# Kernel optimization log

Measured on AMD Instinct MI355X. Metric: run time of the kernel, lower is better.

Reference implementation:

```python
import jax, jax.numpy as jnp
import numpy as np

N, F, D = 4096, 32, 16      # nodes, channels, irrep dim for L<=3 (1+3+5+7)
E = 65536                    # edges (avg degree 16)
S = 64                       # species
R = 8                        # radial basis size
AVG = 16.0                   # avg_num_neighbors
L_SLICES = ((0, 1), (1, 4), (4, 9), (9, 16))   # per-l blocks of the 16-dim irrep axis
IR_OUT_REPS = np.array([1, 3])                 # output irreps 0e (dim 1) + 1o (dim 3)
MIX_REPS = np.array([1, 3, 5, 7])              # per-l scalar mix broadcast over m


def _sph(v):
    # real spherical harmonics l=1..3 of normalized vectors (4pi-normalized), [E,15]
    r2 = jnp.sum(v * v, axis=-1, keepdims=True)
    u = v / jnp.sqrt(jnp.where(r2 == 0.0, 1.0, r2))
    x, y, z = u[:, 0], u[:, 1], u[:, 2]
    s3, s5, s7 = 3.0 ** 0.5, 5.0 ** 0.5, 7.0 ** 0.5
    s15, s42, s70, s105 = 15.0 ** 0.5, 42.0 ** 0.5, 70.0 ** 0.5, 105.0 ** 0.5
    Y1 = [s3 * x, s3 * y, s3 * z]
    Y2 = [s15 * x * y, s15 * y * z, 0.5 * s5 * (3 * z * z - 1), s15 * x * z, 0.5 * s15 * (x * x - y * y)]
    Y3 = [0.25 * s70 * y * (3 * x * x - y * y), s105 * x * y * z, 0.25 * s42 * y * (5 * z * z - 1),
          0.5 * s7 * z * (5 * z * z - 3), 0.25 * s42 * x * (5 * z * z - 1),
          0.5 * s105 * z * (x * x - y * y), 0.25 * s70 * x * (x * x - 3 * y * y)]
    return jnp.stack(Y1 + Y2 + Y3, axis=-1)


def _per_l_linear(xs, W):
    # channel mixing within each l block: xs [N,C,16], W [4,C,Fout] -> [N,Fout,16]
    return jnp.concatenate([jnp.einsum('nci,cf->nfi', xs[:, :, a:b], W[l])
                            for l, (a, b) in enumerate(L_SLICES)], axis=-1)


def setup_inputs() -> dict:
    key = jax.random.key(0)
    ks = jax.random.split(key, 17)
    rs = np.random.RandomState(0)
    # sparse CG-like tensor-product / symmetric-contraction basis tensors (fixed constants)
    cg = (rs.randn(D, 15, D) * (rs.rand(D, 15, D) < 0.08)).astype(np.float32)
    u3 = (rs.randn(D, D, D, 4) * (rs.rand(D, D, D, 4) < 0.05)).astype(np.float32)
    u2 = (rs.randn(D, D, 4) * (rs.rand(D, D, 4) < 0.15)).astype(np.float32)
    u1 = (rs.randn(D, 4) * (rs.rand(D, 4) < 0.4)).astype(np.float32)

    def g(k, shape, s):
        return jax.random.normal(k, shape, dtype=jnp.float32) * s

    return {
        'node_feats': g(ks[0], (N, F, D), 1.0),
        'vectors': g(ks[1], (E, 3), 1.0),
        'radial_embedding': jax.random.uniform(ks[2], (E, R), dtype=jnp.float32),
        'W_up': g(ks[3], (4, F, F), F ** -0.5),
        'CG': jnp.asarray(cg),
        'W_r1': g(ks[4], (R, 64), R ** -0.5),
        'W_r2': g(ks[5], (64, 64), 64 ** -0.5),
        'W_r3': g(ks[6], (64, 64), 64 ** -0.5),
        'W_r4': g(ks[7], (64, 2 * F * 4), 64 ** -0.5),
        'W_down': g(ks[8], (4, 2 * F, F), (2 * F) ** -0.5),
        'U3': jnp.asarray(u3),
        'U2': jnp.asarray(u2),
        'U1': jnp.asarray(u1),
        'w3': g(ks[9], (S, 2, F), 1.0),
        'w2': g(ks[10], (S, 2, F), 1.0),
        'w1': g(ks[11], (S, 2, F), 1.0),
        'W_sc': g(ks[12], (2, S, F, F), F ** -0.5),
        'W_out': g(ks[13], (2, F, F), F ** -0.5),
        'node_species': jax.random.randint(ks[14], (N,), 0, S, dtype=jnp.int32),
        'senders': jax.random.randint(ks[15], (E,), 0, N, dtype=jnp.int32),
        'receivers': jax.random.randint(ks[16], (E,), 0, N, dtype=jnp.int32),
    }


def _forward(node_feats, vectors, radial_embedding, W_up, CG, W_r1, W_r2, W_r3, W_r4,
             W_down, U3, U2, U1, w3, w2, w1, W_sc, W_out,
             node_species, senders, receivers):
    # linear_up
    x = _per_l_linear(node_feats, W_up)                              # [N,F,16]
    # message passing convolution
    fs = x[senders]                                                  # gather [E,F,16]
    Y = _sph(vectors)                                                # [E,15]
    M = jnp.einsum('ej,ijk->eik', Y, CG)                             # per-edge TP operator [E,16,16]
    tp = jnp.einsum('efi,eik->efk', fs, M)                           # [E,F,16]
    msg = jnp.concatenate([fs, tp], axis=1)                          # [E,2F,16]
    h = jax.nn.silu(radial_embedding @ W_r1)
    h = jax.nn.silu(h @ W_r2)
    h = jax.nn.silu(h @ W_r3)
    mix = (h @ W_r4).reshape(E, 2 * F, 4)                            # per-(channel,l) scalar
    mix = jnp.repeat(mix, MIX_REPS, axis=-1, total_repeat_length=D)  # [E,2F,16]
    msg = msg * mix
    agg = jax.ops.segment_sum(msg, receivers, num_segments=N) / jnp.sqrt(AVG)
    y = _per_l_linear(agg, W_down) / jnp.sqrt(AVG)                   # linear_down [N,F,16]
    # symmetric contraction (correlation 3) with species-indexed weights
    def expand(w):  # [S,2,F] -> per-node per-output-irrep-dim scalar [N,F,4]
        return jnp.repeat(jnp.transpose(w[node_species], (0, 2, 1)), IR_OUT_REPS,
                          axis=-1, total_repeat_length=4)
    w3e, w2e, w1e = expand(w3), expand(w2), expand(w1)
    T = jnp.einsum('abji,ncj->ncabi', U3, y) * w3e[:, :, None, None, :]  # [N,F,16,16,4]
    T = T + U2[None, None] * w2e[:, :, None, None, :]
    T = jnp.einsum('ncaji,ncj->ncai', T, y)                              # [N,F,16,4]
    T = T + U1[None, None] * w1e[:, :, None, :]
    B = jnp.einsum('ncji,ncj->nci', T, y)                                # [N,F,4]
    # output linear (per output irrep) + species-indexed skip connection
    o = jnp.concatenate([jnp.einsum('nci,cf->nfi', B[:, :, :1], W_out[0]),
                         jnp.einsum('nci,cf->nfi', B[:, :, 1:4], W_out[1])], axis=-1)
    sc = jnp.concatenate([jnp.einsum('nci,ncf->nfi', x[:, :, :1], W_sc[0][node_species]),
                          jnp.einsum('nci,ncf->nfi', x[:, :, 1:4], W_sc[1][node_species])], axis=-1)
    return (o + sc).reshape(N, F * 4)


def reference(node_feats, vectors, radial_embedding, W_up, CG, W_r1, W_r2, W_r3, W_r4,
              W_down, U3, U2, U1, w3, w2, w1, W_sc, W_out,
              node_species, senders, receivers):
    return _forward(node_feats, vectors, radial_embedding, W_up, CG, W_r1, W_r2, W_r3, W_r4,
                    W_down, U3, U2, U1, w3, w2, w1, W_sc, W_out,
                    node_species, senders, receivers)
```

## Files before the change

kernel.cpp:

```cpp
#include <hip/hip_runtime.h>
#include <math.h>

#define NN 4096
#define FF 32
#define DD 16
#define EE 65536

__device__ __forceinline__ int l_of(int i){ return (i==0)?0:(i<4)?1:(i<9)?2:3; }
__device__ __forceinline__ float silu(float v){ return v/(1.f+expf(-v)); }

__global__ __launch_bounds__(512) void k_x(const float* __restrict__ feats,
        const float* __restrict__ Wup, float* __restrict__ x){
  __shared__ float sF[FF*DD];
  __shared__ float sW[4*FF*FF];
  int n = blockIdx.x, t = threadIdx.x;
  sF[t] = feats[(size_t)n*FF*DD + t];
  for (int k=t;k<4*FF*FF;k+=512) sW[k]=Wup[k];
  __syncthreads();
  int f = t>>4, i = t&15;
  const float* W = &sW[l_of(i)*FF*FF];
  float a=0.f;
  #pragma unroll
  for (int c=0;c<FF;c++) a += sF[c*DD+i]*W[c*FF+f];
  x[(size_t)n*FF*DD + t] = a;
}

__global__ __launch_bounds__(256) void k_Y(const float* __restrict__ vec, float* __restrict__ Yp){
  int e = blockIdx.x*256+threadIdx.x;
  if (e>=EE) return;
  float vx=vec[(size_t)e*3+0], vy=vec[(size_t)e*3+1], vz=vec[(size_t)e*3+2];
  float r2=vx*vx+vy*vy+vz*vz;
  float inv = (r2==0.f)?1.f:rsqrtf(r2);
  float X=vx*inv, Y=vy*inv, Z=vz*inv;
  const float s3=1.7320508075688772f, s5=2.23606797749979f, s7=2.6457513110645907f;
  const float s15=3.872983346207417f, s42=6.48074069840786f, s70=8.366600265340756f, s105=10.246950765959598f;
  float y[16];
  y[0]=s3*X; y[1]=s3*Y; y[2]=s3*Z;
  y[3]=s15*X*Y; y[4]=s15*Y*Z; y[5]=0.5f*s5*(3.f*Z*Z-1.f); y[6]=s15*X*Z; y[7]=0.5f*s15*(X*X-Y*Y);
  y[8]=0.25f*s70*Y*(3.f*X*X-Y*Y); y[9]=s105*X*Y*Z; y[10]=0.25f*s42*Y*(5.f*Z*Z-1.f);
  y[11]=0.5f*s7*Z*(5.f*Z*Z-3.f); y[12]=0.25f*s42*X*(5.f*Z*Z-1.f);
  y[13]=0.5f*s105*Z*(X*X-Y*Y); y[14]=0.25f*s70*X*(X*X-3.f*Y*Y);
  y[15]=0.f;
  #pragma unroll
  for(int q=0;q<4;q++) *(float4*)&Yp[(size_t)e*16+q*4] = *(float4*)&y[q*4];
}

__global__ __launch_bounds__(256) void k_mix(const float* __restrict__ rad,
    const float* __restrict__ W1, const float* __restrict__ W2,
    const float* __restrict__ W3, const float* __restrict__ W4,
    float* __restrict__ mix){
  __shared__ float sRadT[8*68];
  __shared__ float sW1[8*64];
  __shared__ float sHA[64*68];
  __shared__ float sHB[64*68];
  int t = threadIdx.x;
  int be = blockIdx.x*64;
  for (int k=t;k<8*64;k+=256) sW1[k]=W1[k];
  for (int idx=t; idx<64*8; idx+=256){ int e=idx>>3, k=idx&7; sRadT[k*68+e]=rad[(size_t)(be+e)*8+k]; }
  __syncthreads();
  int e0 = (t>>4)*4, j0 = (t&15)*4;
  {
    float acc[4][4];
    #pragma unroll
    for(int a=0;a<4;a++){ acc[a][0]=0;acc[a][1]=0;acc[a][2]=0;acc[a][3]=0; }
    #pragma unroll
    for(int k=0;k<8;k++){
      float4 h = *(const float4*)&sRadT[k*68+e0];
      float4 w = *(const float4*)&sW1[k*64+j0];
      acc[0][0]+=h.x*w.x; acc[0][1]+=h.x*w.y; acc[0][2]+=h.x*w.z; acc[0][3]+=h.x*w.w;
      acc[1][0]+=h.y*w.x; acc[1][1]+=h.y*w.y; acc[1][2]+=h.y*w.z; acc[1][3]+=h.y*w.w;
      acc[2][0]+=h.z*w.x; acc[2][1]+=h.z*w.y; acc[2][2]+=h.z*w.z; acc[2][3]+=h.z*w.w;
      acc[3][0]+=h.w*w.x; acc[3][1]+=h.w*w.y; acc[3][2]+=h.w*w.z; acc[3][3]+=h.w*w.w;
    }
    #pragma unroll
    for(int b=0;b<4;b++){
      float4 v; v.x=silu(acc[0][b]); v.y=silu(acc[1][b]); v.z=silu(acc[2][b]); v.w=silu(acc[3][b]);
      *(float4*)&sHA[(j0+b)*68+e0] = v;
    }
  }
  __syncthreads();
  {
    float acc[4][4];
    #pragma unroll
    for(int a=0;a<4;a++){ acc[a][0]=0;acc[a][1]=0;acc[a][2]=0;acc[a][3]=0; }
    for(int k=0;k<64;k++){
      float4 h = *(const float4*)&sHA[k*68+e0];
      float4 w = *(const float4*)&W2[k*64+j0];
      acc[0][0]+=h.x*w.x; acc[0][1]+=h.x*w.y; acc[0][2]+=h.x*w.z; acc[0][3]+=h.x*w.w;
      acc[1][0]+=h.y*w.x; acc[1][1]+=h.y*w.y; acc[1][2]+=h.y*w.z; acc[1][3]+=h.y*w.w;
      acc[2][0]+=h.z*w.x; acc[2][1]+=h.z*w.y; acc[2][2]+=h.z*w.z; acc[2][3]+=h.z*w.w;
      acc[3][0]+=h.w*w.x; acc[3][1]+=h.w*w.y; acc[3][2]+=h.w*w.z; acc[3][3]+=h.w*w.w;
    }
    #pragma unroll
    for(int b=0;b<4;b++){
      float4 v; v.x=silu(acc[0][b]); v.y=silu(acc[1][b]); v.z=silu(acc[2][b]); v.w=silu(acc[3][b]);
      *(float4*)&sHB[(j0+b)*68+e0] = v;
    }
  }
  __syncthreads();
  {
    float acc[4][4];
    #pragma unroll
    for(int a=0;a<4;a++){ acc[a][0]=0;acc[a][1]=0;acc[a][2]=0;acc[a][3]=0; }
    for(int k=0;k<64;k++){
      float4 h = *(const float4*)&sHB[k*68+e0];
      float4 w = *(const float4*)&W3[k*64+j0];
      acc[0][0]+=h.x*w.x; acc[0][1]+=h.x*w.y; acc[0][2]+=h.x*w.z; acc[0][3]+=h.x*w.w;
      acc[1][0]+=h.y*w.x; acc[1][1]+=h.y*w.y; acc[1][2]+=h.y*w.z; acc[1][3]+=h.y*w.w;
      acc[2][0]+=h.z*w.x; acc[2][1]+=h.z*w.y; acc[2][2]+=h.z*w.z; acc[2][3]+=h.z*w.w;
      acc[3][0]+=h.w*w.x; acc[3][1]+=h.w*w.y; acc[3][2]+=h.w*w.z; acc[3][3]+=h.w*w.w;
    }
    #pragma unroll
    for(int b=0;b<4;b++){
      float4 v; v.x=silu(acc[0][b]); v.y=silu(acc[1][b]); v.z=silu(acc[2][b]); v.w=silu(acc[3][b]);
      *(float4*)&sHA[(j0+b)*68+e0] = v;
    }
  }
  __syncthreads();
  {
    int cc0 = (t&63)*4, g = t>>6;
    float acc[4][4][4];
    #pragma unroll
    for(int r=0;r<4;r++)
      #pragma unroll
      for(int a=0;a<4;a++){ acc[r][a][0]=0;acc[r][a][1]=0;acc[r][a][2]=0;acc[r][a][3]=0; }
    for(int k=0;k<64;k++){
      float4 w = *(const float4*)&W4[k*256+cc0];
      #pragma unroll
      for(int r=0;r<4;r++){
        float4 h = *(const float4*)&sHA[k*68 + (g+4*r)*4];
        acc[r][0][0]+=h.x*w.x; acc[r][0][1]+=h.x*w.y; acc[r][0][2]+=h.x*w.z; acc[r][0][3]+=h.x*w.w;
        acc[r][1][0]+=h.y*w.x; acc[r][1][1]+=h.y*w.y; acc[r][1][2]+=h.y*w.z; acc[r][1][3]+=h.y*w.w;
        acc[r][2][0]+=h.z*w.x; acc[r][2][1]+=h.z*w.y; acc[r][2][2]+=h.z*w.z; acc[r][2][3]+=h.z*w.w;
        acc[r][3][0]+=h.w*w.x; acc[r][3][1]+=h.w*w.y; acc[r][3][2]+=h.w*w.z; acc[r][3][3]+=h.w*w.w;
      }
    }
    #pragma unroll
    for(int r=0;r<4;r++)
      #pragma unroll
      for(int a=0;a<4;a++){
        int e = (g+4*r)*4 + a;
        float4 v; v.x=acc[r][a][0]; v.y=acc[r][a][1]; v.z=acc[r][a][2]; v.w=acc[r][a][3];
        *(float4*)&mix[(size_t)(be+e)*256 + cc0] = v;
      }
  }
}

__global__ void k_zero(int* cnt){ int t=blockIdx.x*256+threadIdx.x; if(t<NN) cnt[t]=0; }
__global__ void k_count(const int* __restrict__ recv, int* cnt, int* pos){
  int e=blockIdx.x*256+threadIdx.x; pos[e]=atomicAdd(&cnt[recv[e]],1); }
__global__ __launch_bounds__(256) void k_scan(const int* __restrict__ cnt, int* __restrict__ off){
  __shared__ int sums[256]; __shared__ int bases[256];
  int t=threadIdx.x;
  int local[16]; int s=0;
  #pragma unroll
  for(int k=0;k<16;k++){ local[k]=cnt[t*16+k]; s+=local[k]; }
  sums[t]=s; __syncthreads();
  if(t==0){ int a=0; for(int q=0;q<256;q++){ bases[q]=a; a+=sums[q]; } }
  __syncthreads();
  int acc=bases[t];
  #pragma unroll
  for(int k=0;k<16;k++){ off[t*16+k]=acc; acc+=local[k]; }
  if(t==255) off[NN]=acc;
}
__global__ void k_fill(const int* __restrict__ recv, const int* __restrict__ off,
                       const int* __restrict__ pos, int* __restrict__ elist){
  int e=blockIdx.x*256+threadIdx.x; elist[off[recv[e]]+pos[e]]=e; }

__global__ __launch_bounds__(256) void k_compact(const float* __restrict__ U3,
    const float* __restrict__ U2, const float* __restrict__ U1,
    int* u3i, float* u3v, int* u2i, float* u2v, int* u1i, float* u1v, int* uoff){
  const float* src; int n; int* oi; float* ov; int slot=blockIdx.x;
  if(slot==0){src=U3;n=16384;oi=u3i;ov=u3v;}
  else if(slot==1){src=U2;n=1024;oi=u2i;ov=u2v;}
  else {src=U1;n=64;oi=u1i;ov=u1v;}
  __shared__ int cnts[256][4]; __shared__ int bases[256][4];
  int t=threadIdx.x;
  int chunk=(n+255)/256;
  int lo=t*chunk, hi=min(n,lo+chunk); if(lo>n) lo=n;
  int c0=0,c1=0,c2=0,c3=0;
  for(int q=lo;q<hi;q++) if(src[q]!=0.f){
    int i=q&3;
    if(i==0)c0++; else if(i==1)c1++; else if(i==2)c2++; else c3++;
  }
  cnts[t][0]=c0; cnts[t][1]=c1; cnts[t][2]=c2; cnts[t][3]=c3;
  __syncthreads();
  if(t==0){
    int a=0;
    for(int i=0;i<4;i++){ uoff[slot*5+i]=a;
      for(int q=0;q<256;q++){ bases[q][i]=a; a+=cnts[q][i]; } }
    uoff[slot*5+4]=a;
  }
  __syncthreads();
  int w0=bases[t][0], w1_=bases[t][1], w2_=bases[t][2], w3_=bases[t][3];
  for(int q=lo;q<hi;q++){ float v=src[q]; if(v!=0.f){
    int i=q&3;
    if(i==0){ oi[w0]=q; ov[w0]=v; w0++; }
    else if(i==1){ oi[w1_]=q; ov[w1_]=v; w1_++; }
    else if(i==2){ oi[w2_]=q; ov[w2_]=v; w2_++; }
    else { oi[w3_]=q; ov[w3_]=v; w3_++; }
  } }
}

__global__ __launch_bounds__(256) void k_gather(
    const float* __restrict__ x, const float* __restrict__ mix,
    const float* __restrict__ Yp, const float* __restrict__ CG,
    const int* __restrict__ senders,
    const int* __restrict__ off, const int* __restrict__ elist,
    float* __restrict__ agg)
{
  __shared__ __align__(16) char smem[22528];
  float* sCG  = (float*)smem;
  float* sMW  = (float*)(smem+15360);
  float* sP   = (float*)smem;
  int*   sEl  = (int*)(smem+19456);
  int*   sEl2 = (int*)(smem+20480);
  int*   sSnd = (int*)(smem+21504);

  int n = blockIdx.x, t = threadIdx.x;
  int w = t>>6, l = t&63, lc = l&31, kh = (l>>5)*8;

  for (int k=t;k<3840;k+=256) sCG[k]=CG[k];
  int base = off[n];
  int deg = off[n+1]-base; if (deg>256) deg=256;
  for (int d=t; d<deg; d+=256) sEl[d]=elist[base+d];
  __syncthreads();
  for (int d=t; d<deg; d+=256){
    int v=sEl[d]; int r=0;
    for(int q=0;q<deg;q++) r += (sEl[q]<v);
    sEl2[r]=v;
  }
  __syncthreads();
  for (int d=t; d<deg; d+=256) sSnd[d]=senders[sEl2[d]];
  __syncthreads();

  float aggF[8], aggT[8];
  #pragma unroll
  for(int j=0;j<8;j++){ aggF[j]=0.f; aggT[j]=0.f; }

  for (int g0=0; g0<deg; g0+=4){
    int d = g0+w;
    if (d<deg){
      int myE = __builtin_amdgcn_readfirstlane(sEl2[d]);
      int snd = __builtin_amdgcn_readfirstlane(sSnd[d]);
      const float* yrow = Yp + (size_t)myE*16;
      const float* mrow = mix + (size_t)myE*256;
      const float* xrow = x + (size_t)snd*512;
      float yv[16];
      #pragma unroll
      for(int q=0;q<4;q++) *(float4*)&yv[q*4] = *(const float4*)&yrow[q*4];
      float4 mixF = *(const float4*)&mrow[lc*4];
      float4 mixT = *(const float4*)&mrow[128 + lc*4];
      float fsv[16];
      #pragma unroll
      for(int q=0;q<4;q++) *(float4*)&fsv[q*4] = *(const float4*)&xrow[lc*16 + q*4];
      int li = l>>4, lk = l&15;
      #pragma unroll
      for(int r=0;r<4;r++){
        int i = r*4+li;
        float m=0.f;
        #pragma unroll
        for(int j=0;j<15;j++) m += yv[j]*sCG[i*240 + j*16 + lk];
        sMW[w*256 + r*64 + l] = m;
      }
      float tp[8];
      #pragma unroll
      for(int j=0;j<8;j++) tp[j]=0.f;
      #pragma unroll
      for(int i=0;i<16;i++){
        float4 ma = *(const float4*)&sMW[w*256 + i*16 + kh];
        float4 mb = *(const float4*)&sMW[w*256 + i*16 + kh + 4];
        float f = fsv[i];
        tp[0]+=f*ma.x; tp[1]+=f*ma.y; tp[2]+=f*ma.z; tp[3]+=f*ma.w;
        tp[4]+=f*mb.x; tp[5]+=f*mb.y; tp[6]+=f*mb.z; tp[7]+=f*mb.w;
      }
      #pragma unroll
      for(int j=0;j<8;j++){
        int k = kh+j;
        int g = l_of(k);
        float mF = (g==0)?mixF.x:(g==1)?mixF.y:(g==2)?mixF.z:mixF.w;
        float mT = (g==0)?mixT.x:(g==1)?mixT.y:(g==2)?mixT.z:mixT.w;
        aggF[j] += fsv[k]*mF;
        aggT[j] += tp[j]*mT;
      }
    }
  }
  __syncthreads();

  #pragma unroll
  for(int j=0;j<8;j++){
    sP[w*1024 + lc*16 + kh + j]       = aggF[j];
    sP[w*1024 + (32+lc)*16 + kh + j]  = aggT[j];
  }
  __syncthreads();
  for (int idx=t; idx<1024; idx+=256)
    agg[(size_t)n*1024 + idx] = sP[idx]+sP[1024+idx]+sP[2048+idx]+sP[3072+idx];
}

__global__ __launch_bounds__(256) void k_tail(
    const float* __restrict__ agg, const float* __restrict__ x,
    const float* __restrict__ Wdown,
    const int* __restrict__ u3i, const float* __restrict__ u3v,
    const int* __restrict__ u2i, const float* __restrict__ u2v,
    const int* __restrict__ u1i, const float* __restrict__ u1v,
    const int* __restrict__ uoff,
    const float* __restrict__ w3, const float* __restrict__ w2,
    const float* __restrict__ w1,
    const float* __restrict__ Wsc, const float* __restrict__ Wout,
    const int* __restrict__ species,
    float* __restrict__ out)
{
  __shared__ float sAgg[2048];
  __shared__ float sy[1024];
  __shared__ float sPart[1024];

  int n0 = blockIdx.x*2, t = threadIdx.x;
  #pragma unroll
  for(int q=0;q<8;q++) sAgg[q*256+t] = agg[(size_t)n0*1024 + q*256 + t];
  __syncthreads();

  {
    int h=t>>7, ii=(t>>3)&15, f0=(t&7)*4;
    const float* W = Wdown + l_of(ii)*2048;
    float ax=0.f, ay=0.f, az=0.f, aw=0.f;
    for(int c=0;c<64;c++){
      float a = sAgg[h*1024 + c*16 + ii];
      float4 wv = *(const float4*)&W[c*32+f0];
      ax+=a*wv.x; ay+=a*wv.y; az+=a*wv.z; aw+=a*wv.w;
    }
    sy[h*512 + ii*32 + f0+0]=ax*0.0625f;
    sy[h*512 + ii*32 + f0+1]=ay*0.0625f;
    sy[h*512 + ii*32 + f0+2]=az*0.0625f;
    sy[h*512 + ii*32 + f0+3]=aw*0.0625f;
  }
  __syncthreads();

  float* sXn = sAgg;
  float* sB  = sAgg + 1024;
  #pragma unroll
  for(int q=0;q<4;q++){ int idx=q*256+t;
    sXn[idx] = x[(size_t)(n0+(idx>>9))*512 + (idx&511)]; }

  {
    int p  = __builtin_amdgcn_readfirstlane(t>>6);
    int c  = t&31, hf=(t>>5)&1;
    int spec = species[n0+hf];
    const float* syc = &sy[hf*512 + c];
    #pragma unroll
    for(int i=0;i<4;i++){
      float r3=0.f;
      for(int q=uoff[i]+p; q<uoff[i+1]; q+=4){
        int id=u3i[q]; float v=u3v[q];
        int a=(id>>10)&15, b=(id>>6)&15, j=(id>>2)&15;
        r3 += v*syc[a*32]*syc[b*32]*syc[j*32];
      }
      float r2=0.f;
      for(int q=uoff[5+i]+p; q<uoff[5+i+1]; q+=4){
        int id=u2i[q]; float v=u2v[q];
        int a=(id>>6)&15, b=(id>>2)&15;
        r2 += v*syc[a*32]*syc[b*32];
      }
      float r1=0.f;
      for(int q=uoff[10+i]+p; q<uoff[10+i+1]; q+=4){
        int id=u1i[q]; float v=u1v[q];
        int a=(id>>2)&15;
        r1 += v*syc[a*32];
      }
      float wa = (i==0)? w3[spec*64+c] : w3[spec*64+32+c];
      float wb = (i==0)? w2[spec*64+c] : w2[spec*64+32+c];
      float wc = (i==0)? w1[spec*64+c] : w1[spec*64+32+c];
      sPart[p*256 + i*64 + hf*32 + c] = r3*wa + r2*wb + r1*wc;
    }
  }
  __syncthreads();

  {
    int hf2=t>>7, c2=(t>>2)&31, i2=t&3;
    int o = i2*64 + hf2*32 + c2;
    sB[hf2*128 + c2*4 + i2] = sPart[o] + sPart[256+o] + sPart[512+o] + sPart[768+o];
  }
  __syncthreads();

  {
    int hf3=t>>7, f=(t>>2)&31, i3=t&3;
    int sp2 = species[n0+hf3];
    int sel = (i3==0)?0:1;
    const float* Wo = Wout + sel*1024;
    const float* Ws = Wsc + (size_t)(sel*64+sp2)*1024;
    float o=0.f, sc=0.f;
    for(int c2=0;c2<32;c2++){
      o  += sB[hf3*128 + c2*4 + i3]*Wo[c2*32+f];
      sc += sXn[hf3*512 + c2*16 + i3]*Ws[c2*32+f];
    }
    out[(size_t)(n0+hf3)*128 + f*4 + i3] = o + sc;
  }
}

extern "C" void kernel_launch(void* const* d_in, const int* in_sizes, int n_in,
                              void* d_out, int out_size, void* d_ws, size_t ws_size,
                              hipStream_t stream){
  (void)in_sizes; (void)n_in; (void)out_size; (void)ws_size;
  const float* feats = (const float*)d_in[0];
  const float* vec   = (const float*)d_in[1];
  const float* rad   = (const float*)d_in[2];
  const float* Wup   = (const float*)d_in[3];
  const float* CG    = (const float*)d_in[4];
  const float* Wr1   = (const float*)d_in[5];
  const float* Wr2   = (const float*)d_in[6];
  const float* Wr3   = (const float*)d_in[7];
  const float* Wr4   = (const float*)d_in[8];
  const float* Wdown = (const float*)d_in[9];
  const float* U3    = (const float*)d_in[10];
  const float* U2    = (const float*)d_in[11];
  const float* U1    = (const float*)d_in[12];
  const float* w3    = (const float*)d_in[13];
  const float* w2    = (const float*)d_in[14];
  const float* w1    = (const float*)d_in[15];
  const float* Wsc   = (const float*)d_in[16];
  const float* Wout  = (const float*)d_in[17];
  const int* species = (const int*)d_in[18];
  const int* senders = (const int*)d_in[19];
  const int* recv    = (const int*)d_in[20];
  float* out = (float*)d_out;

  char* w = (char*)d_ws;
  float* x    = (float*)w;  w += (size_t)NN*512*4;
  float* mix  = (float*)w;  w += (size_t)EE*256*4;
  float* Yp   = (float*)w;  w += (size_t)EE*16*4;
  float* agg  = (float*)w;  w += (size_t)NN*1024*4;
  int* cnt    = (int*)w;    w += (size_t)NN*4;
  int* off    = (int*)w;    w += (size_t)(NN+1)*4;
  int* pos    = (int*)w;    w += (size_t)EE*4;
  int* elist  = (int*)w;    w += (size_t)EE*4;
  int* u3i    = (int*)w;    w += 16384*4;
  float* u3v  = (float*)w;  w += 16384*4;
  int* u2i    = (int*)w;    w += 1024*4;
  float* u2v  = (float*)w;  w += 1024*4;
  int* u1i    = (int*)w;    w += 64*4;
  float* u1v  = (float*)w;  w += 64*4;
  int* uoff   = (int*)w;    w += 16*4;

  k_compact<<<3,256,0,stream>>>(U3,U2,U1,u3i,u3v,u2i,u2v,u1i,u1v,uoff);
  k_x<<<NN,512,0,stream>>>(feats,Wup,x);
  k_Y<<<EE/256,256,0,stream>>>(vec,Yp);
  k_mix<<<EE/64,256,0,stream>>>(rad,Wr1,Wr2,Wr3,Wr4,mix);
  k_zero<<<NN/256,256,0,stream>>>(cnt);
  k_count<<<EE/256,256,0,stream>>>(recv,cnt,pos);
  k_scan<<<1,256,0,stream>>>(cnt,off);
  k_fill<<<EE/256,256,0,stream>>>(recv,off,pos,elist);
  k_gather<<<NN,256,0,stream>>>(x,mix,Yp,CG,senders,off,elist,agg);
  k_tail<<<NN/2,256,0,stream>>>(agg,x,Wdown,u3i,u3v,u2i,u2v,u1i,u1v,uoff,
                                w3,w2,w1,Wsc,Wout,species,out);
}
```

Measured before the change: 315.4 us.

## Write edge data in receiver-sorted order and give each wave its own node in gather

A new sort kernel computes each edge's position in the receiver-sorted, edge-id-ordered list and the sender for that slot. The Y and mix kernels then scatter their outputs into that order, so the gather reads mix and Y rows contiguously. The gather kernel now assigns one node per wavefront (four nodes per block) instead of splitting one node's edges across four waves. This removes the in-block rank sort, the shared-memory reduction and the per-block syncs. The costs are an extra kernel and scattered writes in k_Y and k_mix, and low-degree nodes may leave waves less evenly loaded.

```diff
diff --git a/kernel.cpp b/kernel.cpp
--- a/kernel.cpp
+++ b/kernel.cpp
@@ -25,7 +25,8 @@
   x[(size_t)n*FF*DD + t] = a;
 }
 
-__global__ __launch_bounds__(256) void k_Y(const float* __restrict__ vec, float* __restrict__ Yp){
+__global__ __launch_bounds__(256) void k_Y(const float* __restrict__ vec,
+        const int* __restrict__ epos, float* __restrict__ Yp){
   int e = blockIdx.x*256+threadIdx.x;
   if (e>=EE) return;
   float vx=vec[(size_t)e*3+0], vy=vec[(size_t)e*3+1], vz=vec[(size_t)e*3+2];
@@ -41,14 +42,15 @@
   y[11]=0.5f*s7*Z*(5.f*Z*Z-3.f); y[12]=0.25f*s42*X*(5.f*Z*Z-1.f);
   y[13]=0.5f*s105*Z*(X*X-Y*Y); y[14]=0.25f*s70*X*(X*X-3.f*Y*Y);
   y[15]=0.f;
-  #pragma unroll
-  for(int q=0;q<4;q++) *(float4*)&Yp[(size_t)e*16+q*4] = *(float4*)&y[q*4];
+  size_t ep = (size_t)epos[e];
+  #pragma unroll
+  for(int q=0;q<4;q++) *(float4*)&Yp[ep*16+q*4] = *(float4*)&y[q*4];
 }
 
 __global__ __launch_bounds__(256) void k_mix(const float* __restrict__ rad,
     const float* __restrict__ W1, const float* __restrict__ W2,
     const float* __restrict__ W3, const float* __restrict__ W4,
-    float* __restrict__ mix){
+    const int* __restrict__ epos, float* __restrict__ mix){
   __shared__ float sRadT[8*68];
   __shared__ float sW1[8*64];
   __shared__ float sHA[64*68];
@@ -140,8 +142,9 @@
       #pragma unroll
       for(int a=0;a<4;a++){
         int e = (g+4*r)*4 + a;
+        size_t ep = (size_t)epos[be+e];
         float4 v; v.x=acc[r][a][0]; v.y=acc[r][a][1]; v.z=acc[r][a][2]; v.w=acc[r][a][3];
-        *(float4*)&mix[(size_t)(be+e)*256 + cc0] = v;
+        *(float4*)&mix[ep*256 + cc0] = v;
       }
   }
 }
@@ -166,6 +169,24 @@
 __global__ void k_fill(const int* __restrict__ recv, const int* __restrict__ off,
                        const int* __restrict__ pos, int* __restrict__ elist){
   int e=blockIdx.x*256+threadIdx.x; elist[off[recv[e]]+pos[e]]=e; }
+
+__global__ __launch_bounds__(256) void k_sort(const int* __restrict__ senders,
+    const int* __restrict__ off, const int* __restrict__ elist,
+    int* __restrict__ epos, int* __restrict__ ssend){
+  __shared__ int buf[4][256];
+  int t=threadIdx.x, w=t>>6, l=t&63;
+  int n = blockIdx.x*4 + w;
+  int base = off[n];
+  int deg = off[n+1]-base; if (deg>256) deg=256;
+  for(int d=l; d<deg; d+=64) buf[w][d]=elist[base+d];
+  __syncthreads();
+  for(int d=l; d<deg; d+=64){
+    int v=buf[w][d]; int r=0;
+    for(int q=0;q<deg;q++) r += (buf[w][q]<v);
+    epos[v] = base + r;
+    ssend[base+r] = senders[v];
+  }
+}
 
 __global__ __launch_bounds__(256) void k_compact(const float* __restrict__ U3,
     const float* __restrict__ U2, const float* __restrict__ U1,
@@ -202,99 +223,76 @@
   } }
 }
 
-__global__ __launch_bounds__(256) void k_gather(
-    const float* __restrict__ x, const float* __restrict__ mix,
-    const float* __restrict__ Yp, const float* __restrict__ CG,
-    const int* __restrict__ senders,
-    const int* __restrict__ off, const int* __restrict__ elist,
+__global__ __launch_bounds__(256,6) void k_gather(
+    const float* __restrict__ x, const float* __restrict__ mix_s,
+    const float* __restrict__ Yp_s, const float* __restrict__ CG,
+    const int* __restrict__ off, const int* __restrict__ ssend,
     float* __restrict__ agg)
 {
-  __shared__ __align__(16) char smem[22528];
-  float* sCG  = (float*)smem;
-  float* sMW  = (float*)(smem+15360);
-  float* sP   = (float*)smem;
-  int*   sEl  = (int*)(smem+19456);
-  int*   sEl2 = (int*)(smem+20480);
-  int*   sSnd = (int*)(smem+21504);
-
-  int n = blockIdx.x, t = threadIdx.x;
-  int w = t>>6, l = t&63, lc = l&31, kh = (l>>5)*8;
-
+  __shared__ float sCG[3840];
+  __shared__ float sMW[4][256];
+  int t=threadIdx.x, w=t>>6, l=t&63, lc=l&31, kh=(l>>5)*8;
+  int li=l>>4, lk=l&15;
   for (int k=t;k<3840;k+=256) sCG[k]=CG[k];
-  int base = off[n];
-  int deg = off[n+1]-base; if (deg>256) deg=256;
-  for (int d=t; d<deg; d+=256) sEl[d]=elist[base+d];
-  __syncthreads();
-  for (int d=t; d<deg; d+=256){
-    int v=sEl[d]; int r=0;
-    for(int q=0;q<deg;q++) r += (sEl[q]<v);
-    sEl2[r]=v;
-  }
-  __syncthreads();
-  for (int d=t; d<deg; d+=256) sSnd[d]=senders[sEl2[d]];
+  int n = __builtin_amdgcn_readfirstlane(blockIdx.x*4 + w);
+  int base = __builtin_amdgcn_readfirstlane(off[n]);
+  int deg  = __builtin_amdgcn_readfirstlane(off[n+1]) - base;
+  if (deg>256) deg=256;
   __syncthreads();
 
   float aggF[8], aggT[8];
   #pragma unroll
   for(int j=0;j<8;j++){ aggF[j]=0.f; aggT[j]=0.f; }
 
-  for (int g0=0; g0<deg; g0+=4){
-    int d = g0+w;
-    if (d<deg){
-      int myE = __builtin_amdgcn_readfirstlane(sEl2[d]);
-      int snd = __builtin_amdgcn_readfirstlane(sSnd[d]);
-      const float* yrow = Yp + (size_t)myE*16;
-      const float* mrow = mix + (size_t)myE*256;
-      const float* xrow = x + (size_t)snd*512;
-      float yv[16];
+  for (int d=0; d<deg; ++d){
+    int slot = base+d;
+    int snd = __builtin_amdgcn_readfirstlane(ssend[slot]);
+    const float* mrow = mix_s + (size_t)slot*256;
+    const float* xrow = x + (size_t)snd*512;
+    const float* yrow = Yp_s + (size_t)slot*16;
+    float4 mixF = *(const float4*)&mrow[lc*4];
+    float4 mixT = *(const float4*)&mrow[128 + lc*4];
+    float fsv[16];
+    #pragma unroll
+    for(int q=0;q<4;q++) *(float4*)&fsv[q*4] = *(const float4*)&xrow[lc*16 + q*4];
+    float yv[16];
+    #pragma unroll
+    for(int q=0;q<16;q++) yv[q]=yrow[q];
+    #pragma unroll
+    for(int r=0;r<4;r++){
+      int i = r*4+li;
+      float m=0.f;
       #pragma unroll
-      for(int q=0;q<4;q++) *(float4*)&yv[q*4] = *(const float4*)&yrow[q*4];
-      float4 mixF = *(const float4*)&mrow[lc*4];
-      float4 mixT = *(const float4*)&mrow[128 + lc*4];
-      float fsv[16];
-      #pragma unroll
-      for(int q=0;q<4;q++) *(float4*)&fsv[q*4] = *(const float4*)&xrow[lc*16 + q*4];
-      int li = l>>4, lk = l&15;
-      #pragma unroll
-      for(int r=0;r<4;r++){
-        int i = r*4+li;
-        float m=0.f;
-        #pragma unroll
-        for(int j=0;j<15;j++) m += yv[j]*sCG[i*240 + j*16 + lk];
-        sMW[w*256 + r*64 + l] = m;
-      }
-      float tp[8];
-      #pragma unroll
-      for(int j=0;j<8;j++) tp[j]=0.f;
-      #pragma unroll
-      for(int i=0;i<16;i++){
-        float4 ma = *(const float4*)&sMW[w*256 + i*16 + kh];
-        float4 mb = *(const float4*)&sMW[w*256 + i*16 + kh + 4];
-        float f = fsv[i];
-        tp[0]+=f*ma.x; tp[1]+=f*ma.y; tp[2]+=f*ma.z; tp[3]+=f*ma.w;
-        tp[4]+=f*mb.x; tp[5]+=f*mb.y; tp[6]+=f*mb.z; tp[7]+=f*mb.w;
-      }
-      #pragma unroll
-      for(int j=0;j<8;j++){
-        int k = kh+j;
-        int g = l_of(k);
-        float mF = (g==0)?mixF.x:(g==1)?mixF.y:(g==2)?mixF.z:mixF.w;
-        float mT = (g==0)?mixT.x:(g==1)?mixT.y:(g==2)?mixT.z:mixT.w;
-        aggF[j] += fsv[k]*mF;
-        aggT[j] += tp[j]*mT;
-      }
-    }
-  }
-  __syncthreads();
-
-  #pragma unroll
-  for(int j=0;j<8;j++){
-    sP[w*1024 + lc*16 + kh + j]       = aggF[j];
-    sP[w*1024 + (32+lc)*16 + kh + j]  = aggT[j];
-  }
-  __syncthreads();
-  for (int idx=t; idx<1024; idx+=256)
-    agg[(size_t)n*1024 + idx] = sP[idx]+sP[1024+idx]+sP[2048+idx]+sP[3072+idx];
+      for(int j=0;j<15;j++) m += yv[j]*sCG[i*240 + j*16 + lk];
+      sMW[w][r*64 + l] = m;
+    }
+    float tp[8];
+    #pragma unroll
+    for(int j=0;j<8;j++) tp[j]=0.f;
+    #pragma unroll
+    for(int i=0;i<16;i++){
+      float4 ma = *(const float4*)&sMW[w][i*16 + kh];
+      float4 mb = *(const float4*)&sMW[w][i*16 + kh + 4];
+      float f = fsv[i];
+      tp[0]+=f*ma.x; tp[1]+=f*ma.y; tp[2]+=f*ma.z; tp[3]+=f*ma.w;
+      tp[4]+=f*mb.x; tp[5]+=f*mb.y; tp[6]+=f*mb.z; tp[7]+=f*mb.w;
+    }
+    #pragma unroll
+    for(int j=0;j<8;j++){
+      int k = kh+j;
+      int g = l_of(k);
+      float mF = (g==0)?mixF.x:(g==1)?mixF.y:(g==2)?mixF.z:mixF.w;
+      float mT = (g==0)?mixT.x:(g==1)?mixT.y:(g==2)?mixT.z:mixT.w;
+      aggF[j] += fsv[k]*mF;
+      aggT[j] += tp[j]*mT;
+    }
+  }
+
+  float* aout = agg + (size_t)n*1024;
+  *(float4*)&aout[lc*16+kh]        = *(float4*)&aggF[0];
+  *(float4*)&aout[lc*16+kh+4]      = *(float4*)&aggF[4];
+  *(float4*)&aout[(32+lc)*16+kh]   = *(float4*)&aggT[0];
+  *(float4*)&aout[(32+lc)*16+kh+4] = *(float4*)&aggT[4];
 }
 
 __global__ __launch_bounds__(256) void k_tail(
@@ -432,6 +430,8 @@
   int* off    = (int*)w;    w += (size_t)(NN+1)*4;
   int* pos    = (int*)w;    w += (size_t)EE*4;
   int* elist  = (int*)w;    w += (size_t)EE*4;
+  int* epos   = (int*)w;    w += (size_t)EE*4;
+  int* ssend  = (int*)w;    w += (size_t)EE*4;
   int* u3i    = (int*)w;    w += 16384*4;
   float* u3v  = (float*)w;  w += 16384*4;
   int* u2i    = (int*)w;    w += 1024*4;
@@ -442,13 +442,14 @@
 
   k_compact<<<3,256,0,stream>>>(U3,U2,U1,u3i,u3v,u2i,u2v,u1i,u1v,uoff);
   k_x<<<NN,512,0,stream>>>(feats,Wup,x);
-  k_Y<<<EE/256,256,0,stream>>>(vec,Yp);
-  k_mix<<<EE/64,256,0,stream>>>(rad,Wr1,Wr2,Wr3,Wr4,mix);
   k_zero<<<NN/256,256,0,stream>>>(cnt);
   k_count<<<EE/256,256,0,stream>>>(recv,cnt,pos);
   k_scan<<<1,256,0,stream>>>(cnt,off);
   k_fill<<<EE/256,256,0,stream>>>(recv,off,pos,elist);
-  k_gather<<<NN,256,0,stream>>>(x,mix,Yp,CG,senders,off,elist,agg);
+  k_sort<<<NN/4,256,0,stream>>>(senders,off,elist,epos,ssend);
+  k_Y<<<EE/256,256,0,stream>>>(vec,epos,Yp);
+  k_mix<<<EE/64,256,0,stream>>>(rad,Wr1,Wr2,Wr3,Wr4,epos,mix);
+  k_gather<<<NN/4,256,0,stream>>>(x,mix,Yp,CG,off,ssend,agg);
   k_tail<<<NN/2,256,0,stream>>>(agg,x,Wdown,u3i,u3v,u2i,u2v,u1i,u1v,uoff,
                                 w3,w2,w1,Wsc,Wout,species,out);
 }
```

Measured after the change: 442.8 us. 1.4x slower.
